# Performance work log

Measured on AMD Instinct MI355X. Metric: run time of the kernel, lower is better.

The kernel has to match this reference:

```python
import math
import jax, jax.numpy as jnp
import numpy as np

FACTOR = math.pi ** (-0.5)
C1 = math.sqrt(3.0 / 8.0) * FACTOR
C2 = math.sqrt(3.0 / 4.0) * FACTOR
EPS = 1e-9


def _cg_111():
    # Clebsch-Gordan <1 m1 ; 1 m2 | 1 m3>, indexed [m1+1, m2+1, m3+1]
    s = 1.0 / math.sqrt(2.0)
    cg = np.zeros((3, 3, 3), np.float32)
    cg[2, 1, 2] = s   # <1,1;1,0|1,1>
    cg[1, 2, 2] = -s  # <1,0;1,1|1,1>
    cg[2, 0, 1] = s   # <1,1;1,-1|1,0>
    cg[0, 2, 1] = -s  # <1,-1;1,1|1,0>
    cg[1, 0, 0] = s   # <1,0;1,-1|1,-1>
    cg[0, 1, 0] = -s  # <1,-1;1,0|1,-1>
    return jnp.asarray(cg)


def spherical_l1(r):
    # r: [n,p,q,3] -> Y1, Y2: [n,p,q,3] (real/imag parts of Y_1^m)
    rx, ry, rz = r[..., 0], r[..., 1], r[..., 2]
    Y1 = jnp.stack([C1 * rx, C2 * rz, -C1 * rx], axis=-1)
    Y2 = jnp.stack([-C1 * ry, jnp.zeros_like(ry), -C1 * ry], axis=-1)
    zero = (jnp.linalg.norm(r, axis=-1) == 0.0)[..., None]
    Y1 = jnp.where(zero, 1.0, Y1)
    Y2 = jnp.where(zero, 1.0, Y2)
    return Y1, Y2


def setup_inputs() -> dict:
    key = jax.random.key(0)
    ks = jax.random.split(key, 12)
    n, p, fr, fin, fout = 16, 256, 64, 64, 64
    rbf = jax.random.normal(ks[0], (n, p, p, fr), jnp.float32)
    uv = jax.random.normal(ks[1], (n, p, p, 3), jnp.float32)
    uv = uv / (jnp.linalg.norm(uv, axis=-1, keepdims=True) + 1e-12)
    inp1 = jax.random.normal(ks[2], (n, p, 3, fin), jnp.float32)
    inp2 = jax.random.normal(ks[3], (n, p, 3, fin), jnp.float32)
    mask = jnp.ones((n, p), jnp.bool_)
    sc = 0.08
    W1 = jax.random.normal(ks[4], (fin, fr), jnp.float32) * sc
    b1 = jax.random.normal(ks[5], (fin,), jnp.float32) * sc
    W2 = jax.random.normal(ks[6], (fin, fin), jnp.float32) * sc
    b2 = jax.random.normal(ks[7], (fin,), jnp.float32) * sc
    W_si = jax.random.normal(ks[8], (fout, fin), jnp.float32) * sc
    bias_b = jax.random.normal(ks[9], (1,), jnp.float32) * sc
    return {"rbf": rbf, "unit_vector": uv, "inp1": inp1, "inp2": inp2,
            "mask": mask, "coef": _cg_111(), "W1": W1, "b1": b1,
            "W2": W2, "b2": b2, "W_si": W_si, "bias_b": bias_b}


def reference(rbf, unit_vector, inp1, inp2, mask, coef, W1, b1, W2, b2, W_si, bias_b):
    m = mask[:, :, None, None]  # broadcast over q and last dims
    Y1, Y2 = spherical_l1(unit_vector)
    Y1 = jnp.where(m, Y1, 0.0)
    Y2 = jnp.where(m, Y2, 0.0)
    # radial embedding MLP: Linear -> ReLU -> Linear
    radial = jnp.einsum('npqr,fr->npqf', rbf, W1) + b1
    radial = jax.nn.relu(radial)
    radial = jnp.einsum('npqf,gf->npqg', radial, W2) + b2
    radial = jnp.where(m, radial, 0.0)

    def tp(Y, inp):
        return jnp.einsum('abc,npqb,npqf,npaf->nqcf', coef, Y, radial, inp,
                          optimize='optimal')

    out1 = tp(Y1, inp1) - tp(Y2, inp2)
    out2 = tp(Y2, inp1) + tp(Y1, inp2)
    # norm over {stack, c} dims, keepdim on c -> [n,q,1,f]
    norm = jnp.sqrt(jnp.sum(out1 ** 2 + out2 ** 2, axis=-2, keepdims=True))
    out1 = out1 / (norm + EPS)
    out2 = out2 / (norm + EPS)
    # gated self-interaction
    out1 = jnp.einsum('nqcf,gf->nqcg', out1, W_si)
    out2 = jnp.einsum('nqcf,gf->nqcg', out2, W_si)
    norm2 = jnp.sqrt(jnp.sum(out1 ** 2 + out2 ** 2, axis=-2))  # [n,q,g]
    nonlinear = jax.nn.relu(norm2 + bias_b[0])[:, :, None, :]  # [n,q,1,g]
    return out1 * nonlinear, out2 * nonlinear
```

## Files before the change

kernel.cpp:

```cpp
#include <hip/hip_runtime.h>
#include <hip/hip_bf16.h>

typedef __attribute__((ext_vector_type(8))) short short8;
typedef __attribute__((ext_vector_type(4))) float f32x4;
typedef __attribute__((ext_vector_type(4))) unsigned int u32x4;

#define MFMA16(A, B, C) __builtin_amdgcn_mfma_f32_16x16x32_bf16(A, B, C, 0, 0, 0)

__device__ __forceinline__ unsigned int pkbf(float lo, float hi) {
  unsigned int ul = (unsigned int)__bfloat16_as_ushort(__float2bfloat16(lo));
  unsigned int uh = (unsigned int)__bfloat16_as_ushort(__float2bfloat16(hi));
  return ul | (uh << 16);
}

union S8U { short8 s; u32x4 u; };
__device__ __forceinline__ short8 mk8(unsigned int a, unsigned int b,
                                      unsigned int c, unsigned int d) {
  S8U t; u32x4 v = {a, b, c, d}; t.u = v; return t.s;
}

constexpr float SU = 0.24430125595146f;
constexpr float SW = 0.34549414947134f;


__global__ __launch_bounds__(256) void tfield_partial(
    const float* __restrict__ rbf,  const float* __restrict__ uv,
    const float* __restrict__ inp1, const float* __restrict__ inp2,
    const float* __restrict__ W1,   const float* __restrict__ b1,
    const float* __restrict__ W2,   const float* __restrict__ b2,
    float* __restrict__ ws)
{
  __shared__ __align__(16) unsigned char pool[27008];
  unsigned int* wfrag = (unsigned int*)pool;
  unsigned int* hbuf  = (unsigned int*)(pool + 12288);
  float* ibuf  = (float*)(pool + 20480);
  float* biasL = (float*)(pool + 26624);
  float* accL  = (float*)pool;

  const int tid = threadIdx.x;
  const int l   = tid & 63;
  const int w   = tid >> 6;
  const int g   = l >> 4;
  const int qh  = l & 15;
  const int bid = blockIdx.x;
  const int nq  = bid >> 2;
  const int fh  = (bid >> 1) & 1;
  const int ph  = bid & 1;
  const int n   = nq >> 4;
  const int q0  = (nq & 15) << 4;

  #pragma unroll
  for (int k = 0; k < 3; ++k) {
    const int slot = tid + (k << 8);
    const int fi = slot >> 6;
    const int ll = slot & 63;
    const int gg = ll >> 4;
    const int qq = ll & 15;
    const float* src;
    if (fi < 8) {
      src = W1 + ((fi >> 1) * 16 + qq) * 64 + (fi & 1) * 32 + gg * 8;
    } else {
      const int fj = fi - 8;
      src = W2 + (((fh << 1) + (fj >> 1)) * 16 + qq) * 64 + (fj & 1) * 32 + gg * 8;
    }
    f32x4 x0 = *(const f32x4*)src;
    f32x4 x1 = *(const f32x4*)(src + 4);
    u32x4 vv = {pkbf(x0[0], x0[1]), pkbf(x0[2], x0[3]), pkbf(x1[0], x1[1]), pkbf(x1[2], x1[3])};
    *(u32x4*)(wfrag + ((fi << 6) + ll) * 4) = vv;
  }
  if (tid < 96) biasL[tid] = (tid < 64) ? b1[tid] : b2[(fh << 5) + tid - 64];
  __syncthreads();

  const float* bL1 = biasL;
  const float* bL2 = biasL + 64;

  f32x4 accT[2][6];
  #pragma unroll
  for (int a = 0; a < 2; ++a)
    #pragma unroll
    for (int j = 0; j < 6; ++j) accT[a][j] = (f32x4){0.f, 0.f, 0.f, 0.f};

  const size_t nbase = (size_t)n * 256;
  const int pbase = (ph << 7) + w;

  const int sl = (l < 24) ? l : l - 24;
  const float* isrcb = (l < 24) ? inp1 : inp2;
  const int ioff = (sl >> 3) * 64 + (fh << 5) + ((sl & 7) << 2);

  unsigned int* hrow = hbuf + (w << 9) + (qh << 5);
  float* iw = ibuf + w * 384;
  const int swz = qh & 7;

  f32x4 rn0, rn1, rn2, rn3;
  { const float* rr = rbf + ((nbase + pbase) * 256 + q0 + qh) * 64 + (g << 3);
    rn0 = *(const f32x4*)rr;        rn1 = *(const f32x4*)(rr + 4);
    rn2 = *(const f32x4*)(rr + 32); rn3 = *(const f32x4*)(rr + 36); }
  f32x4 stage_v = {0.f, 0.f, 0.f, 0.f};
  if (l < 48) stage_v = *(const f32x4*)(isrcb + (nbase + pbase) * 192 + ioff);
  float uc0, uc1, uc2, un0, un1, un2;
  { const float* u = uv + ((nbase + pbase) * 256 + q0 + qh) * 3;
    uc0 = u[0]; uc1 = u[1]; uc2 = u[2]; }

  short8 rf0 = mk8(pkbf(rn0[0], rn0[1]), pkbf(rn0[2], rn0[3]), pkbf(rn1[0], rn1[1]), pkbf(rn1[2], rn1[3]));
  short8 rf1 = mk8(pkbf(rn2[0], rn2[1]), pkbf(rn2[2], rn2[3]), pkbf(rn3[0], rn3[1]), pkbf(rn3[2], rn3[3]));
  f32x4 h4[4];
  #pragma unroll
  for (int mt = 0; mt < 4; ++mt) {
    f32x4 c = *(const f32x4*)(bL1 + (mt << 4) + (g << 2));
    short8 a0 = *(const short8*)(wfrag + (((mt << 1) + 0) * 64 + l) * 4);
    short8 a1 = *(const short8*)(wfrag + (((mt << 1) + 1) * 64 + l) * 4);
    c = MFMA16(a0, rf0, c);
    c = MFMA16(a1, rf1, c);
    h4[mt] = c;
  }
  if (l < 48) *(f32x4*)(iw + (l << 2)) = stage_v;
  #pragma unroll
  for (int mt = 0; mt < 4; ++mt) {
    const float e0 = fmaxf(h4[mt][0], 0.f);
    const float e1 = fmaxf(h4[mt][1], 0.f);
    const float e2 = fmaxf(h4[mt][2], 0.f);
    const float e3 = fmaxf(h4[mt][3], 0.f);
    const int base = ((((mt << 1) + (g >> 1)) ^ swz) << 2) + ((g & 1) << 1);
    hrow[base]     = pkbf(e0, e1);
    hrow[base + 1] = pkbf(e2, e3);
  }
  short8 hb0 = *(const short8*)(hrow + (((0 + g) ^ swz) << 2));
  short8 hb1 = *(const short8*)(hrow + (((4 + g) ^ swz) << 2));
  { const float* rr = rbf + ((nbase + pbase + 4) * 256 + q0 + qh) * 64 + (g << 3);
    rn0 = *(const f32x4*)rr;        rn1 = *(const f32x4*)(rr + 4);
    rn2 = *(const f32x4*)(rr + 32); rn3 = *(const f32x4*)(rr + 36); }
  if (l < 48) stage_v = *(const f32x4*)(isrcb + (nbase + pbase + 4) * 192 + ioff);
  { const float* u = uv + ((nbase + pbase + 4) * 256 + q0 + qh) * 3;
    un0 = u[0]; un1 = u[1]; un2 = u[2]; }

  for (int s = 0; s < 32; ++s) {
    const int s2 = (s + 2 < 32) ? s + 2 : 31;

    rf0 = mk8(pkbf(rn0[0], rn0[1]), pkbf(rn0[2], rn0[3]), pkbf(rn1[0], rn1[1]), pkbf(rn1[2], rn1[3]));
    rf1 = mk8(pkbf(rn2[0], rn2[1]), pkbf(rn2[2], rn2[3]), pkbf(rn3[0], rn3[1]), pkbf(rn3[2], rn3[3]));
    #pragma unroll
    for (int mt = 0; mt < 4; ++mt) {
      f32x4 c = *(const f32x4*)(bL1 + (mt << 4) + (g << 2));
      short8 a0 = *(const short8*)(wfrag + (((mt << 1) + 0) * 64 + l) * 4);
      short8 a1 = *(const short8*)(wfrag + (((mt << 1) + 1) * 64 + l) * 4);
      c = MFMA16(a0, rf0, c);
      c = MFMA16(a1, rf1, c);
      h4[mt] = c;
    }
    { const float* rr = rbf + ((nbase + pbase + (s2 << 2)) * 256 + q0 + qh) * 64 + (g << 3);
      rn0 = *(const f32x4*)rr;        rn1 = *(const f32x4*)(rr + 4);
      rn2 = *(const f32x4*)(rr + 32); rn3 = *(const f32x4*)(rr + 36); }

    f32x4 cc0, cc1;
    {
      f32x4 c = *(const f32x4*)(bL2 + (g << 2));
      short8 wa0 = *(const short8*)(wfrag + ((8 + 0) * 64 + l) * 4);
      short8 wa1 = *(const short8*)(wfrag + ((8 + 1) * 64 + l) * 4);
      c = MFMA16(wa0, hb0, c);
      c = MFMA16(wa1, hb1, c);
      cc0 = c;
      c = *(const f32x4*)(bL2 + 16 + (g << 2));
      wa0 = *(const short8*)(wfrag + ((8 + 2) * 64 + l) * 4);
      wa1 = *(const short8*)(wfrag + ((8 + 3) * 64 + l) * 4);
      c = MFMA16(wa0, hb0, c);
      c = MFMA16(wa1, hb1, c);
      cc1 = c;
    }

    const float su  = SU * uc0;
    const float sv  = SU * uc1;
    const float swc = SW * uc2;
    uc0 = un0; uc1 = un1; uc2 = un2;
    { const float* u = uv + ((nbase + pbase + (s2 << 2)) * 256 + q0 + qh) * 3;
      un0 = u[0]; un1 = u[1]; un2 = u[2]; }

    const float* ib = iw + ((s & 1) * 192) + (g << 2);
    #pragma unroll
    for (int mt2l = 0; mt2l < 2; ++mt2l) {
      const f32x4 A0 = *(const f32x4*)(ib + (mt2l << 4));
      const f32x4 A1 = *(const f32x4*)(ib + (mt2l << 4) + 32);
      const f32x4 A2 = *(const f32x4*)(ib + (mt2l << 4) + 64);
      const f32x4 B0 = *(const f32x4*)(ib + (mt2l << 4) + 96);
      const f32x4 B1 = *(const f32x4*)(ib + (mt2l << 4) + 128);
      const f32x4 B2 = *(const f32x4*)(ib + (mt2l << 4) + 160);
      const f32x4 cc = mt2l ? cc1 : cc0;

      const f32x4 t1 = su * A1, t2 = sv * B1;
      const f32x4 t3 = su * B1, t4 = sv * A1;
      const f32x4 g10 = (t1 + t2) - swc * A0;
      const f32x4 g11 = su * (A0 + A2) - sv * (B0 - B2);
      const f32x4 g12 = (t1 - t2) + swc * A2;
      const f32x4 g20 = (t3 - t4) - swc * B0;
      const f32x4 g21 = sv * (A0 - A2) + su * (B0 + B2);
      const f32x4 g22 = (t3 + t4) + swc * B2;
      accT[mt2l][0] += cc * g10;
      accT[mt2l][1] += cc * g11;
      accT[mt2l][2] += cc * g12;
      accT[mt2l][3] += cc * g20;
      accT[mt2l][4] += cc * g21;
      accT[mt2l][5] += cc * g22;
    }

    if (l < 48) *(f32x4*)(iw + (((s + 1) & 1) * 192) + (l << 2)) = stage_v;
    if (l < 48) stage_v = *(const f32x4*)(isrcb + (nbase + pbase + (s2 << 2)) * 192 + ioff);

    #pragma unroll
    for (int mt = 0; mt < 4; ++mt) {
      const float e0 = fmaxf(h4[mt][0], 0.f);
      const float e1 = fmaxf(h4[mt][1], 0.f);
      const float e2 = fmaxf(h4[mt][2], 0.f);
      const float e3 = fmaxf(h4[mt][3], 0.f);
      const int base = ((((mt << 1) + (g >> 1)) ^ swz) << 2) + ((g & 1) << 1);
      hrow[base]     = pkbf(e0, e1);
      hrow[base + 1] = pkbf(e2, e3);
    }
    hb0 = *(const short8*)(hrow + (((0 + g) ^ swz) << 2));
    hb1 = *(const short8*)(hrow + (((4 + g) ^ swz) << 2));
  }

  __syncthreads();
  for (int i = tid; i < 3072; i += 256) accL[i] = 0.f;
  __syncthreads();
  for (int t = 0; t < 4; ++t) {
    if (w == t) {
      #pragma unroll
      for (int mt2l = 0; mt2l < 2; ++mt2l)
        #pragma unroll
        for (int v = 0; v < 4; ++v) {
          float* dst = accL + (((qh << 5) + (mt2l << 4) + (g << 2) + v) * 6);
          #pragma unroll
          for (int j = 0; j < 6; ++j) dst[j] += accT[mt2l][j][v];
        }
    }
    __syncthreads();
  }
  float* wp = ws + (size_t)bid * 3072;
  for (int i = tid; i < 3072; i += 256) wp[i] = accL[i];
}

__global__ __launch_bounds__(512) void tfield_finish(
    const float* __restrict__ ws, const float* __restrict__ Wsi,
    const float* __restrict__ biasb, float* __restrict__ out)
{
  __shared__ __align__(16) float accL[6144];
  __shared__ __align__(16) float wsiT[4096];

  const int tid = threadIdx.x;
  const int l   = tid & 63;
  const int w   = tid >> 6;
  const int nq  = blockIdx.x;
  const int n   = nq >> 4;
  const int q0  = (nq & 15) << 4;

  const float* c00 = ws + (size_t)(nq * 4 + 0) * 3072;
  const float* c01 = c00 + 3072;
  const float* c10 = c00 + 6144;
  const float* c11 = c00 + 9216;
  for (int i = tid; i < 3072; i += 512) {
    const int qhh = i / 192;
    const int rem = i - qhh * 192;
    accL[qhh * 384 + rem]       = c00[i] + c01[i];
    accL[qhh * 384 + 192 + rem] = c10[i] + c11[i];
  }
  #pragma unroll
  for (int k = 0; k < 8; ++k) {
    const int f = (w << 3) + k;
    wsiT[(f << 6) + l] = Wsi[(l << 6) + f];
  }
  __syncthreads();

  #pragma unroll
  for (int rep = 0; rep < 2; ++rep) {
    const int qq = w + (rep << 3);
    float* xp = accL + ((qq << 6) + l) * 6;
    const float x0 = xp[0], x1 = xp[1], x2 = xp[2], x3 = xp[3], x4 = xp[4], x5 = xp[5];
    const float nrm = sqrtf(x0*x0 + x1*x1 + x2*x2 + x3*x3 + x4*x4 + x5*x5);
    const float sc = 1.f / (nrm + 1e-9f);
    xp[0] = x0 * sc; xp[1] = x1 * sc; xp[2] = x2 * sc;
    xp[3] = x3 * sc; xp[4] = x4 * sc; xp[5] = x5 * sc;
  }
  __syncthreads();

  const float bb = biasb[0];
  #pragma unroll
  for (int rep = 0; rep < 2; ++rep) {
    const int qq = w + (rep << 3);
    const float* arow = accL + (qq << 6) * 6;
    float pj0 = 0, pj1 = 0, pj2 = 0, pj3 = 0, pj4 = 0, pj5 = 0;
    for (int f = 0; f < 64; ++f) {
      const float wv = wsiT[(f << 6) + l];
      const float* ap = arow + f * 6;
      pj0 += ap[0] * wv; pj1 += ap[1] * wv; pj2 += ap[2] * wv;
      pj3 += ap[3] * wv; pj4 += ap[4] * wv; pj5 += ap[5] * wv;
    }
    const float s2 = pj0*pj0 + pj1*pj1 + pj2*pj2 + pj3*pj3 + pj4*pj4 + pj5*pj5;
    const float nl = fmaxf(sqrtf(s2) + bb, 0.f);
    const int q = q0 + qq;
    float* o1 = out + (size_t)((n * 256 + q) * 3) * 64 + l;
    float* o2 = o1 + 786432;
    o1[0]   = pj0 * nl;
    o1[64]  = pj1 * nl;
    o1[128] = pj2 * nl;
    o2[0]   = pj3 * nl;
    o2[64]  = pj4 * nl;
    o2[128] = pj5 * nl;
  }
}

__global__ __launch_bounds__(512) void tfield_kernel(
    const float* __restrict__ rbf,  const float* __restrict__ uv,
    const float* __restrict__ inp1, const float* __restrict__ inp2,
    const float* __restrict__ W1,   const float* __restrict__ b1,
    const float* __restrict__ W2,   const float* __restrict__ b2,
    const float* __restrict__ Wsi,  const float* __restrict__ biasb,
    float* __restrict__ out)
{
  __shared__ __align__(16) unsigned char pool[40960];
  unsigned int* wfrag = (unsigned int*)pool;
  unsigned int* hbuf  = (unsigned int*)(pool + 16384);
  float* accL = (float*)pool;
  float* wsiT = (float*)(pool + 24576);

  const int tid = threadIdx.x;
  const int l   = tid & 63;
  const int w   = tid >> 6;
  const int g   = l >> 4;
  const int qh  = l & 15;
  const int n   = blockIdx.x >> 4;
  const int q0  = (blockIdx.x & 15) << 4;

  {
    const int row = ((w >> 1) << 4) + qh;
    const int kb  = ((w & 1) << 5) + (g << 3);
    const float* s1 = W1 + row * 64 + kb;
    f32x4 x0 = *(const f32x4*)s1;
    f32x4 x1 = *(const f32x4*)(s1 + 4);
    u32x4 v1 = {pkbf(x0[0], x0[1]), pkbf(x0[2], x0[3]), pkbf(x1[0], x1[1]), pkbf(x1[2], x1[3])};
    *(u32x4*)(wfrag + ((w << 6) + l) * 4) = v1;
    const float* s2 = W2 + row * 64 + kb;
    x0 = *(const f32x4*)s2;
    x1 = *(const f32x4*)(s2 + 4);
    u32x4 v2 = {pkbf(x0[0], x0[1]), pkbf(x0[2], x0[3]), pkbf(x1[0], x1[1]), pkbf(x1[2], x1[3])};
    *(u32x4*)(wfrag + (((8 + w) << 6) + l) * 4) = v2;
  }
  __syncthreads();

  float accT[4][4][6];
  #pragma unroll
  for (int a = 0; a < 4; ++a)
    #pragma unroll
    for (int b = 0; b < 4; ++b)
      #pragma unroll
      for (int j = 0; j < 6; ++j) accT[a][b][j] = 0.f;

  const size_t nbase = (size_t)n * 256;
  const float* rr0 = rbf + ((nbase + w) * 256 + q0 + qh) * 64 + (g << 3);
  f32x4 nx0 = *(const f32x4*)(rr0);
  f32x4 nx1 = *(const f32x4*)(rr0 + 4);
  f32x4 nx2 = *(const f32x4*)(rr0 + 32);
  f32x4 nx3 = *(const f32x4*)(rr0 + 36);

  unsigned int* hrow = hbuf + ((w << 4) + qh) * 32;
  const int swz = qh & 7;

  for (int s = 0; s < 32; ++s) {
    const int p = (s << 3) + w;
    f32x4 r0 = nx0, r1 = nx1, r2 = nx2, r3 = nx3;
    {
      const int pn = (s < 31) ? p + 8 : p;
      const float* rr = rbf + ((nbase + pn) * 256 + q0 + qh) * 64 + (g << 3);
      nx0 = *(const f32x4*)(rr);
      nx1 = *(const f32x4*)(rr + 4);
      nx2 = *(const f32x4*)(rr + 32);
      nx3 = *(const f32x4*)(rr + 36);
    }
    const float* uvp = uv + ((nbase + p) * 256 + q0 + qh) * 3;
    const float su = SU * uvp[0];
    const float sv = SU * uvp[1];
    const float swc = SW * uvp[2];

    const short8 rf0 = mk8(pkbf(r0[0], r0[1]), pkbf(r0[2], r0[3]), pkbf(r1[0], r1[1]), pkbf(r1[2], r1[3]));
    const short8 rf1 = mk8(pkbf(r2[0], r2[1]), pkbf(r2[2], r2[3]), pkbf(r3[0], r3[1]), pkbf(r3[2], r3[3]));

    f32x4 h4[4];
    #pragma unroll
    for (int mt = 0; mt < 4; ++mt) {
      f32x4 c = *(const f32x4*)(b1 + (mt << 4) + (g << 2));
      short8 a0 = *(const short8*)(wfrag + (((mt << 1) + 0) * 64 + l) * 4);
      short8 a1 = *(const short8*)(wfrag + (((mt << 1) + 1) * 64 + l) * 4);
      c = MFMA16(a0, rf0, c);
      c = MFMA16(a1, rf1, c);
      h4[mt] = c;
    }
    #pragma unroll
    for (int mt = 0; mt < 4; ++mt) {
      const float e0 = fmaxf(h4[mt][0], 0.f);
      const float e1 = fmaxf(h4[mt][1], 0.f);
      const float e2 = fmaxf(h4[mt][2], 0.f);
      const float e3 = fmaxf(h4[mt][3], 0.f);
      const int base = ((((mt << 1) + (g >> 1)) ^ swz) << 2) + ((g & 1) << 1);
      hrow[base]     = pkbf(e0, e1);
      hrow[base + 1] = pkbf(e2, e3);
    }
    const short8 hb0 = *(const short8*)(hrow + (((0 + g) ^ swz) << 2));
    const short8 hb1 = *(const short8*)(hrow + (((4 + g) ^ swz) << 2));

    const float* i1p = inp1 + (nbase + p) * 192 + (g << 2);
    const float* i2p = inp2 + (nbase + p) * 192 + (g << 2);

    #pragma unroll
    for (int mt2 = 0; mt2 < 4; ++mt2) {
      f32x4 c = *(const f32x4*)(b2 + (mt2 << 4) + (g << 2));
      short8 wa0 = *(const short8*)(wfrag + ((8 + (mt2 << 1) + 0) * 64 + l) * 4);
      short8 wa1 = *(const short8*)(wfrag + ((8 + (mt2 << 1) + 1) * 64 + l) * 4);
      c = MFMA16(wa0, hb0, c);
      c = MFMA16(wa1, hb1, c);

      const int fo = mt2 << 4;
      const f32x4 A0 = *(const f32x4*)(i1p + fo);
      const f32x4 A1 = *(const f32x4*)(i1p + fo + 64);
      const f32x4 A2 = *(const f32x4*)(i1p + fo + 128);
      const f32x4 B0 = *(const f32x4*)(i2p + fo);
      const f32x4 B1 = *(const f32x4*)(i2p + fo + 64);
      const f32x4 B2 = *(const f32x4*)(i2p + fo + 128);
      const f32x4 a02p = A0 + A2, a02m = A0 - A2;
      const f32x4 b02p = B0 + B2, b02m = B0 - B2;

      #pragma unroll
      for (int v = 0; v < 4; ++v) {
        const float R = c[v];
        const float pua1 = su * A1[v], pvb1 = sv * B1[v];
        const float pub1 = su * B1[v], pva1 = sv * A1[v];
        const float g10 = pua1 - swc * A0[v] + pvb1;
        const float g11 = su * a02p[v] - sv * b02m[v];
        const float g12 = swc * A2[v] + pua1 - pvb1;
        const float g20 = pub1 - swc * B0[v] - pva1;
        const float g21 = sv * a02m[v] + su * b02p[v];
        const float g22 = swc * B2[v] + pub1 + pva1;
        accT[mt2][v][0] += R * g10;
        accT[mt2][v][1] += R * g11;
        accT[mt2][v][2] += R * g12;
        accT[mt2][v][3] += R * g20;
        accT[mt2][v][4] += R * g21;
        accT[mt2][v][5] += R * g22;
      }
    }
  }

  __syncthreads();
  for (int i = tid; i < 16 * 64 * 6; i += 512) accL[i] = 0.f;
  #pragma unroll
  for (int k = 0; k < 8; ++k) {
    const int f = (w << 3) + k;
    wsiT[(f << 6) + l] = Wsi[(l << 6) + f];
  }
  __syncthreads();

  for (int t = 0; t < 8; ++t) {
    if (w == t) {
      #pragma unroll
      for (int mt2 = 0; mt2 < 4; ++mt2)
        #pragma unroll
        for (int v = 0; v < 4; ++v) {
          float* dst = accL + (((qh << 6) + (mt2 << 4) + (g << 2) + v) * 6);
          #pragma unroll
          for (int j = 0; j < 6; ++j) dst[j] += accT[mt2][v][j];
        }
    }
    __syncthreads();
  }

  #pragma unroll
  for (int rep = 0; rep < 2; ++rep) {
    const int qq = w + (rep << 3);
    float* xp = accL + ((qq << 6) + l) * 6;
    const float x0 = xp[0], x1 = xp[1], x2 = xp[2], x3 = xp[3], x4 = xp[4], x5 = xp[5];
    const float nrm = sqrtf(x0*x0 + x1*x1 + x2*x2 + x3*x3 + x4*x4 + x5*x5);
    const float sc = 1.f / (nrm + 1e-9f);
    xp[0] = x0 * sc; xp[1] = x1 * sc; xp[2] = x2 * sc;
    xp[3] = x3 * sc; xp[4] = x4 * sc; xp[5] = x5 * sc;
  }
  __syncthreads();

  const float bb = biasb[0];
  #pragma unroll
  for (int rep = 0; rep < 2; ++rep) {
    const int qq = w + (rep << 3);
    const float* arow = accL + (qq << 6) * 6;
    float pj0 = 0, pj1 = 0, pj2 = 0, pj3 = 0, pj4 = 0, pj5 = 0;
    for (int f = 0; f < 64; ++f) {
      const float wv = wsiT[(f << 6) + l];
      const float* ap = arow + f * 6;
      pj0 += ap[0] * wv; pj1 += ap[1] * wv; pj2 += ap[2] * wv;
      pj3 += ap[3] * wv; pj4 += ap[4] * wv; pj5 += ap[5] * wv;
    }
    const float s2 = pj0*pj0 + pj1*pj1 + pj2*pj2 + pj3*pj3 + pj4*pj4 + pj5*pj5;
    const float nl = fmaxf(sqrtf(s2) + bb, 0.f);
    const int q = q0 + qq;
    float* o1 = out + (size_t)((n * 256 + q) * 3) * 64 + l;
    float* o2 = o1 + 786432;
    o1[0]   = pj0 * nl;
    o1[64]  = pj1 * nl;
    o1[128] = pj2 * nl;
    o2[0]   = pj3 * nl;
    o2[64]  = pj4 * nl;
    o2[128] = pj5 * nl;
  }
}

extern "C" void kernel_launch(void* const* d_in, const int* in_sizes, int n_in,
                              void* d_out, int out_size, void* d_ws, size_t ws_size,
                              hipStream_t stream) {
  (void)in_sizes; (void)n_in; (void)out_size;
  const size_t ws_needed = (size_t)1024 * 3072 * sizeof(float);
  if (ws_size >= ws_needed) {
    tfield_partial<<<dim3(1024), dim3(256), 0, stream>>>(
        (const float*)d_in[0], (const float*)d_in[1],
        (const float*)d_in[2], (const float*)d_in[3],
        (const float*)d_in[6], (const float*)d_in[7],
        (const float*)d_in[8], (const float*)d_in[9],
        (float*)d_ws);
    tfield_finish<<<dim3(256), dim3(512), 0, stream>>>(
        (const float*)d_ws, (const float*)d_in[10],
        (const float*)d_in[11], (float*)d_out);
  } else {
    tfield_kernel<<<dim3(256), dim3(512), 0, stream>>>(
        (const float*)d_in[0], (const float*)d_in[1],
        (const float*)d_in[2], (const float*)d_in[3],
        (const float*)d_in[6], (const float*)d_in[7],
        (const float*)d_in[8], (const float*)d_in[9],
        (const float*)d_in[10], (const float*)d_in[11],
        (float*)d_out);
  }
}
```

Baseline: 139.5 us.

## Stream rbf and input tiles via direct global-to-LDS async loads

Replaces register-staged prefetching of rbf and inp tiles with global_load_lds direct-to-LDS asynchronous copies into per-wave double-buffered slots, gated by explicit vmcnt waits. The goal is to free VGPRs and hide global load latency further ahead (rbf prefetched three steps ahead), removing the register round trip that staged inputs into LDS. In exchange LDS use grows from about 27KB to about 60KB, which may reduce occupancy, and correctness depends on the hand-tuned vmcnt count with per-wave buffer reuse and no barrier.

Result: slower. 143.2 us (+2.6%).

```diff
diff --git a/kernel.cpp b/kernel.cpp
--- a/kernel.cpp
+++ b/kernel.cpp
@@ -17,6 +17,12 @@
 __device__ __forceinline__ short8 mk8(unsigned int a, unsigned int b,
                                       unsigned int c, unsigned int d) {
   S8U t; u32x4 v = {a, b, c, d}; t.u = v; return t.s;
+}
+
+__device__ __forceinline__ void gload16(const void* g, void* l) {
+  __builtin_amdgcn_global_load_lds(
+      (const __attribute__((address_space(1))) void*)g,
+      (__attribute__((address_space(3))) void*)l, 16, 0, 0);
 }
 
 constexpr float SU = 0.24430125595146f;
@@ -30,11 +36,10 @@
     const float* __restrict__ W2,   const float* __restrict__ b2,
     float* __restrict__ ws)
 {
-  __shared__ __align__(16) unsigned char pool[27008];
+  __shared__ __align__(16) unsigned char pool[59904];
   unsigned int* wfrag = (unsigned int*)pool;
   unsigned int* hbuf  = (unsigned int*)(pool + 12288);
-  float* ibuf  = (float*)(pool + 20480);
-  float* biasL = (float*)(pool + 26624);
+  float* biasL = (float*)(pool + 59392);
   float* accL  = (float*)pool;
 
   const int tid = threadIdx.x;
@@ -88,22 +93,30 @@
   const int ioff = (sl >> 3) * 64 + (fh << 5) + ((sl & 7) << 2);
 
   unsigned int* hrow = hbuf + (w << 9) + (qh << 5);
-  float* iw = ibuf + w * 384;
   const int swz = qh & 7;
 
-  f32x4 rn0, rn1, rn2, rn3;
-  { const float* rr = rbf + ((nbase + pbase) * 256 + q0 + qh) * 64 + (g << 3);
-    rn0 = *(const f32x4*)rr;        rn1 = *(const f32x4*)(rr + 4);
-    rn2 = *(const f32x4*)(rr + 32); rn3 = *(const f32x4*)(rr + 36); }
-  f32x4 stage_v = {0.f, 0.f, 0.f, 0.f};
-  if (l < 48) stage_v = *(const f32x4*)(isrcb + (nbase + pbase) * 192 + ioff);
+  unsigned char* rslot0 = pool + 20480 + (w << 12);
+  unsigned char* rslot1 = rslot0 + 16384;
+  unsigned char* islot0 = pool + 53248 + w * 768;
+  unsigned char* islot1 = islot0 + 3072;
+
+  #define RBF_G(step) (rbf + ((nbase + pbase + ((step) << 2)) * 256 + q0 + qh) * 64 + (g << 3))
+  #define INP_G(step) (isrcb + (nbase + pbase + ((step) << 2)) * 192 + ioff)
+  #define UV_G(step)  (uv + ((nbase + pbase + ((step) << 2)) * 256 + q0 + qh) * 3)
+
   float uc0, uc1, uc2, un0, un1, un2;
-  { const float* u = uv + ((nbase + pbase) * 256 + q0 + qh) * 3;
-    uc0 = u[0]; uc1 = u[1]; uc2 = u[2]; }
-
-  short8 rf0 = mk8(pkbf(rn0[0], rn0[1]), pkbf(rn0[2], rn0[3]), pkbf(rn1[0], rn1[1]), pkbf(rn1[2], rn1[3]));
-  short8 rf1 = mk8(pkbf(rn2[0], rn2[1]), pkbf(rn2[2], rn2[3]), pkbf(rn3[0], rn3[1]), pkbf(rn3[2], rn3[3]));
+  { const float* u = UV_G(0); uc0 = u[0]; uc1 = u[1]; uc2 = u[2]; }
+  { const float* u = UV_G(1); un0 = u[0]; un1 = u[1]; un2 = u[2]; }
+
   f32x4 h4[4];
+  short8 rf0, rf1;
+  {
+    const float* rr = RBF_G(0);
+    f32x4 r0 = *(const f32x4*)rr;        f32x4 r1 = *(const f32x4*)(rr + 4);
+    f32x4 r2 = *(const f32x4*)(rr + 32); f32x4 r3 = *(const f32x4*)(rr + 36);
+    rf0 = mk8(pkbf(r0[0], r0[1]), pkbf(r0[2], r0[3]), pkbf(r1[0], r1[1]), pkbf(r1[2], r1[3]));
+    rf1 = mk8(pkbf(r2[0], r2[1]), pkbf(r2[2], r2[3]), pkbf(r3[0], r3[1]), pkbf(r3[2], r3[3]));
+  }
   #pragma unroll
   for (int mt = 0; mt < 4; ++mt) {
     f32x4 c = *(const f32x4*)(bL1 + (mt << 4) + (g << 2));
@@ -113,7 +126,6 @@
     c = MFMA16(a1, rf1, c);
     h4[mt] = c;
   }
-  if (l < 48) *(f32x4*)(iw + (l << 2)) = stage_v;
   #pragma unroll
   for (int mt = 0; mt < 4; ++mt) {
     const float e0 = fmaxf(h4[mt][0], 0.f);
@@ -126,18 +138,31 @@
   }
   short8 hb0 = *(const short8*)(hrow + (((0 + g) ^ swz) << 2));
   short8 hb1 = *(const short8*)(hrow + (((4 + g) ^ swz) << 2));
-  { const float* rr = rbf + ((nbase + pbase + 4) * 256 + q0 + qh) * 64 + (g << 3);
-    rn0 = *(const f32x4*)rr;        rn1 = *(const f32x4*)(rr + 4);
-    rn2 = *(const f32x4*)(rr + 32); rn3 = *(const f32x4*)(rr + 36); }
-  if (l < 48) stage_v = *(const f32x4*)(isrcb + (nbase + pbase + 4) * 192 + ioff);
-  { const float* u = uv + ((nbase + pbase + 4) * 256 + q0 + qh) * 3;
-    un0 = u[0]; un1 = u[1]; un2 = u[2]; }
+
+  { const float* gp = RBF_G(1);
+    gload16(gp, rslot1); gload16(gp + 4, rslot1 + 1024);
+    gload16(gp + 32, rslot1 + 2048); gload16(gp + 36, rslot1 + 3072); }
+  if (l < 48) gload16(INP_G(0), islot0);
+  { const float* gp = RBF_G(2);
+    gload16(gp, rslot0); gload16(gp + 4, rslot0 + 1024);
+    gload16(gp + 32, rslot0 + 2048); gload16(gp + 36, rslot0 + 3072); }
+  if (l < 48) gload16(INP_G(1), islot1);
 
   for (int s = 0; s < 32; ++s) {
-    const int s2 = (s + 2 < 32) ? s + 2 : 31;
-
-    rf0 = mk8(pkbf(rn0[0], rn0[1]), pkbf(rn0[2], rn0[3]), pkbf(rn1[0], rn1[1]), pkbf(rn1[2], rn1[3]));
-    rf1 = mk8(pkbf(rn2[0], rn2[1]), pkbf(rn2[2], rn2[3]), pkbf(rn3[0], rn3[1]), pkbf(rn3[2], rn3[3]));
+    asm volatile("s_waitcnt vmcnt(5)" ::: "memory");
+    __builtin_amdgcn_sched_barrier(0);
+
+    unsigned char* rslot = ((s + 1) & 1) ? rslot1 : rslot0;
+    unsigned char* islot = (s & 1) ? islot1 : islot0;
+
+    {
+      f32x4 r0 = *(const f32x4*)(rslot + l * 16);
+      f32x4 r1 = *(const f32x4*)(rslot + 1024 + l * 16);
+      f32x4 r2 = *(const f32x4*)(rslot + 2048 + l * 16);
+      f32x4 r3 = *(const f32x4*)(rslot + 3072 + l * 16);
+      rf0 = mk8(pkbf(r0[0], r0[1]), pkbf(r0[2], r0[3]), pkbf(r1[0], r1[1]), pkbf(r1[2], r1[3]));
+      rf1 = mk8(pkbf(r2[0], r2[1]), pkbf(r2[2], r2[3]), pkbf(r3[0], r3[1]), pkbf(r3[2], r3[3]));
+    }
     #pragma unroll
     for (int mt = 0; mt < 4; ++mt) {
       f32x4 c = *(const f32x4*)(bL1 + (mt << 4) + (g << 2));
@@ -147,9 +172,6 @@
       c = MFMA16(a1, rf1, c);
       h4[mt] = c;
     }
-    { const float* rr = rbf + ((nbase + pbase + (s2 << 2)) * 256 + q0 + qh) * 64 + (g << 3);
-      rn0 = *(const f32x4*)rr;        rn1 = *(const f32x4*)(rr + 4);
-      rn2 = *(const f32x4*)(rr + 32); rn3 = *(const f32x4*)(rr + 36); }
 
     f32x4 cc0, cc1;
     {
@@ -171,10 +193,10 @@
     const float sv  = SU * uc1;
     const float swc = SW * uc2;
     uc0 = un0; uc1 = un1; uc2 = un2;
-    { const float* u = uv + ((nbase + pbase + (s2 << 2)) * 256 + q0 + qh) * 3;
-      un0 = u[0]; un1 = u[1]; un2 = u[2]; }
-
-    const float* ib = iw + ((s & 1) * 192) + (g << 2);
+    { const int s2 = (s + 2 < 32) ? s + 2 : 31;
+      const float* u = UV_G(s2); un0 = u[0]; un1 = u[1]; un2 = u[2]; }
+
+    const float* ib = (const float*)islot + (g << 2);
     #pragma unroll
     for (int mt2l = 0; mt2l < 2; ++mt2l) {
       const f32x4 A0 = *(const f32x4*)(ib + (mt2l << 4));
@@ -201,9 +223,6 @@
       accT[mt2l][5] += cc * g22;
     }
 
-    if (l < 48) *(f32x4*)(iw + (((s + 1) & 1) * 192) + (l << 2)) = stage_v;
-    if (l < 48) stage_v = *(const f32x4*)(isrcb + (nbase + pbase + (s2 << 2)) * 192 + ioff);
-
     #pragma unroll
     for (int mt = 0; mt < 4; ++mt) {
       const float e0 = fmaxf(h4[mt][0], 0.f);
@@ -216,7 +235,18 @@
     }
     hb0 = *(const short8*)(hrow + (((0 + g) ^ swz) << 2));
     hb1 = *(const short8*)(hrow + (((4 + g) ^ swz) << 2));
-  }
+
+    __builtin_amdgcn_sched_barrier(0);
+    const int sr = (s + 3 < 32) ? s + 3 : 31;
+    const int si = (s + 2 < 32) ? s + 2 : 31;
+    { const float* gp = RBF_G(sr);
+      gload16(gp, rslot); gload16(gp + 4, rslot + 1024);
+      gload16(gp + 32, rslot + 2048); gload16(gp + 36, rslot + 3072); }
+    if (l < 48) gload16(INP_G(si), islot);
+  }
+  #undef RBF_G
+  #undef INP_G
+  #undef UV_G
 
   __syncthreads();
   for (int i = tid; i < 3072; i += 256) accL[i] = 0.f;
```
